# Kernel optimization log

Hardware: AMD Instinct MI355X
Metric: run time of the kernel (lower is better)

## Reference

```python
import jax, jax.numpy as jnp
import numpy as np
from jax import lax

NEG = -1e16  # value used by masked_fill in the original
DN = ('NCHW', 'OIHW', 'NCHW')


def _time_block(X, w1, b1, w2, b2, w3, b3):
    # X: [B, N, T, C] -> conv over time with kernel (1,3), VALID -> [B, N, T-2, O]
    x = jnp.transpose(X, (0, 3, 1, 2))  # [B, C, N, T]
    conv = lambda w, b: lax.conv_general_dilated(x, w, (1, 1), 'VALID', dimension_numbers=DN) + b[None, :, None, None]
    temp = conv(w1, b1) + jax.nn.sigmoid(conv(w2, b2))
    out = jax.nn.relu(temp + conv(w3, b3))
    return jnp.transpose(out, (0, 2, 3, 1))  # [B, N, T-2, O]


def _gat_single(x, graph, W, b):
    # x: [B, N, C]; W: [D, C]; b: [D]
    h = jnp.einsum('bnc,dc->bnd', x, W)
    s = jnp.einsum('bnd,bmd->bnm', h, h) * graph[None]
    s = jnp.where(s == 0, NEG, s)
    a = jax.nn.softmax(s, axis=-1)
    return jnp.einsum('bnm,bmd->bnd', a, h) + b


def _gat_multihead(x, graph, Wh, bh):
    # x: [B, N, C]; Wh: [H, D, C]; bh: [H, D] -> [B, N, H*D] (head-major concat, matching torch.cat)
    h = jnp.einsum('bnc,hdc->bhnd', x, Wh)
    s = jnp.einsum('bhnd,bhmd->bhnm', h, h) * graph[None, None]
    s = jnp.where(s == 0, NEG, s)
    a = jax.nn.softmax(s, axis=-1)
    o = jnp.einsum('bhnm,bhmd->bhnd', a, h) + bh[None, :, None, :]
    B, H, N, D = o.shape
    return jnp.transpose(o, (0, 2, 1, 3)).reshape(B, N, H * D)


def setup_inputs() -> dict:
    key = jax.random.key(0)
    ks = jax.random.split(key, 12)
    B, N, T, C = 2, 4096, 5, 192
    hid, out_c, H = 64, 64, 4
    inp = {
        'flow': jax.random.normal(ks[0], (B, N, T, C), jnp.float32),
        'graph': jax.random.randint(ks[1], (N, N), 0, 2).astype(jnp.float32),
        'tb_w1': jax.random.normal(ks[2], (hid, C, 1, 3), jnp.float32) * 0.1,
        'tb_b1': jax.random.normal(ks[3], (hid,), jnp.float32) * 0.1,
        'tb_w2': jax.random.normal(ks[4], (hid, C, 1, 3), jnp.float32) * 0.1,
        'tb_b2': jax.random.normal(ks[5], (hid,), jnp.float32) * 0.1,
        'tb_w3': jax.random.normal(ks[6], (hid, C, 1, 3), jnp.float32) * 0.1,
        'tb_b3': jax.random.normal(ks[7], (hid,), jnp.float32) * 0.1,
        'Wh': jax.random.normal(ks[8], (H, hid, C), jnp.float32) * 0.1,
        'bh': jax.random.normal(ks[9], (H, hid), jnp.float32) * 0.1,
        'Wo': jax.random.normal(ks[10], (out_c, hid * H), jnp.float32) * 0.1,
        'bo': jax.random.normal(ks[11], (out_c,), jnp.float32) * 0.1,
    }
    return inp


def reference(flow, graph, tb_w1, tb_b1, tb_w2, tb_b2, tb_w3, tb_b3, Wh, bh, Wo, bo):
    B, N = flow.shape[0], flow.shape[1]
    t1 = _time_block(flow, tb_w1, tb_b1, tb_w2, tb_b2, tb_w3, tb_b3)  # [B, N, T-2, hid]
    x = t1.reshape(B, N, -1)  # [B, N, (T-2)*hid]
    x = jax.nn.leaky_relu(_gat_multihead(x, graph, Wh, bh), negative_slope=0.01)
    x = jax.nn.leaky_relu(_gat_single(x, graph, Wo, bo), negative_slope=0.01)
    return x[:, :, None, :]  # [B, N, 1, out_c]
```

## Files before the change

### kernel.cpp

```cpp
#include <hip/hip_runtime.h>
#include <math.h>

#define N_NODES 4096

typedef unsigned short u16;
typedef unsigned int u32;

typedef __attribute__((ext_vector_type(8))) short bfrag;
typedef __attribute__((ext_vector_type(4))) float f4;

__device__ __forceinline__ u16 f2bf(float x) {
    union { float f; u32 u; } v; v.f = x;
    u32 r = (v.u + 0x7FFFu + ((v.u >> 16) & 1u)) >> 16;
    return (u16)r;
}
__device__ __forceinline__ float bf2f(u16 b) {
    union { float f; u32 u; } v; v.u = ((u32)b) << 16; return v.f;
}
__device__ __forceinline__ u32 cvtpk(float a, float b) {
    u32 r;
    asm("v_cvt_pk_bf16_f32 %0, %1, %2" : "=v"(r) : "v"(a), "v"(b));
    return r;
}
__device__ __forceinline__ float u2f(u32 u) {
    union { u32 u; float f; } v; v.u = u; return v.f;
}
__device__ __forceinline__ float fexp2(float x) {
    float r;
    asm("v_exp_f32 %0, %1" : "=v"(r) : "v"(x));
    return r;
}

#define LOG2E 1.4426950408889634f

__global__ __launch_bounds__(256) void wprep_kernel(
    const float* __restrict__ w1, const float* __restrict__ w2,
    const float* __restrict__ w3,
    u16* __restrict__ w_hi, u16* __restrict__ w_mid, u16* __restrict__ w_lo)
{
    int idx = blockIdx.x * 256 + threadIdx.x;
    if (idx >= 192 * 576) return;
    int col = idx / 576, k = idx % 576;
    int conv = col >> 6, o = col & 63;
    int kk = k / 192, c = k % 192;
    const float* w = (conv == 0) ? w1 : (conv == 1 ? w2 : w3);
    float v = w[(o * 192 + c) * 3 + kk];
    u16 h = f2bf(v);   float r1 = v - bf2f(h);
    u16 m = f2bf(r1);  float r2 = r1 - bf2f(m);
    u16 lo = f2bf(r2);
    int kc = k >> 6, rem = k & 63, j = rem >> 3, e = rem & 7;
    int pos = col * 576 + kc * 64 + ((j ^ (col & 7)) << 3) + e;
    w_hi[pos] = h;
    w_mid[pos] = m;
    w_lo[pos] = lo;
}

__global__ __launch_bounds__(512) void timeblock_mfma_kernel(
    const float* __restrict__ flow,
    const u16* __restrict__ w_hi, const u16* __restrict__ w_mid,
    const u16* __restrict__ w_lo,
    const float* __restrict__ b1, const float* __restrict__ b2,
    const float* __restrict__ b3, float* __restrict__ x1)
{
    __shared__ __align__(16) u16 As[3][128 * 64];
    __shared__ __align__(16) u16 Bs[3][192 * 64];

    const int tid = threadIdx.x;
    const int wv = tid >> 6, l = tid & 63;
    const int ln15 = l & 15, ln16 = l >> 4;
    const int wr = wv >> 1, wc = wv & 1;
    const int nodebase = blockIdx.x * 128;
    const int t = blockIdx.y;

    f4 acc[2][6];
#pragma unroll
    for (int rq = 0; rq < 2; ++rq)
#pragma unroll
        for (int nt = 0; nt < 6; ++nt) {
            acc[rq][nt][0] = 0.f; acc[rq][nt][1] = 0.f;
            acc[rq][nt][2] = 0.f; acc[rq][nt][3] = 0.f;
        }

    for (int kc = 0; kc < 9; ++kc) {
        __syncthreads();

#pragma unroll
        for (int u = tid; u < 1024; u += 512) {
            int r = u >> 3, j = u & 7;
            const float* srcp = flow + (size_t)(nodebase + r) * 960 + t * 192 + kc * 64 + j * 8;
            float4 f0 = *(const float4*)srcp;
            float4 f1 = *(const float4*)(srcp + 4);
            float fv[8] = { f0.x, f0.y, f0.z, f0.w, f1.x, f1.y, f1.z, f1.w };
            union { uint4 q; u16 a[8]; } uh, um, ul;
#pragma unroll
            for (int e = 0; e < 8; ++e) {
                u16 h = f2bf(fv[e]);   float r1 = fv[e] - bf2f(h);
                u16 m = f2bf(r1);      float r2 = r1 - bf2f(m);
                uh.a[e] = h; um.a[e] = m; ul.a[e] = f2bf(r2);
            }
            int pos = r * 64 + ((j ^ (r & 7)) << 3);
            *(uint4*)&As[0][pos] = uh.q;
            *(uint4*)&As[1][pos] = um.q;
            *(uint4*)&As[2][pos] = ul.q;
        }

#pragma unroll
        for (int arr = 0; arr < 3; ++arr) {
            const u16* wsrc = (arr == 0) ? w_hi : (arr == 1 ? w_mid : w_lo);
#pragma unroll
            for (int i = 0; i < 3; ++i) {
                int colg = wv * 24 + i * 8;
                const u16* srcp = wsrc + (size_t)(colg + (l >> 3)) * 576 + kc * 64 + (l & 7) * 8;
                u16* dstp = &Bs[arr][colg * 64];
                __builtin_amdgcn_global_load_lds(
                    (const __attribute__((address_space(1))) u32*)srcp,
                    (__attribute__((address_space(3))) u32*)dstp, 16, 0, 0);
            }
        }

        __syncthreads();

        bfrag af[2][3][2];
#pragma unroll
        for (int rq = 0; rq < 2; ++rq) {
            int arow = wr * 32 + rq * 16 + ln15;
#pragma unroll
            for (int ks = 0; ks < 2; ++ks) {
                int idx = arow * 64 + (((ks * 4 + ln16) ^ (arow & 7)) << 3);
                af[rq][0][ks] = *(const bfrag*)&As[0][idx];
                af[rq][1][ks] = *(const bfrag*)&As[1][idx];
                af[rq][2][ks] = *(const bfrag*)&As[2][idx];
            }
        }

#pragma unroll
        for (int cv = 0; cv < 3; ++cv) {
#pragma unroll
            for (int ntj = 0; ntj < 2; ++ntj) {
                int col = cv * 64 + wc * 32 + ntj * 16 + ln15;
                int nt = cv * 2 + ntj;
#pragma unroll
                for (int ks = 0; ks < 2; ++ks) {
                    int idx = col * 64 + (((ks * 4 + ln16) ^ (col & 7)) << 3);
                    bfrag bh = *(const bfrag*)&Bs[0][idx];
                    bfrag bm = *(const bfrag*)&Bs[1][idx];
                    bfrag bl = *(const bfrag*)&Bs[2][idx];
#pragma unroll
                    for (int rq = 0; rq < 2; ++rq) {
                        f4 a = acc[rq][nt];
                        a = __builtin_amdgcn_mfma_f32_16x16x32_bf16(af[rq][0][ks], bh, a, 0, 0, 0);
                        a = __builtin_amdgcn_mfma_f32_16x16x32_bf16(af[rq][0][ks], bm, a, 0, 0, 0);
                        a = __builtin_amdgcn_mfma_f32_16x16x32_bf16(af[rq][1][ks], bh, a, 0, 0, 0);
                        a = __builtin_amdgcn_mfma_f32_16x16x32_bf16(af[rq][0][ks], bl, a, 0, 0, 0);
                        a = __builtin_amdgcn_mfma_f32_16x16x32_bf16(af[rq][2][ks], bh, a, 0, 0, 0);
                        a = __builtin_amdgcn_mfma_f32_16x16x32_bf16(af[rq][1][ks], bm, a, 0, 0, 0);
                        acc[rq][nt] = a;
                    }
                }
            }
        }
    }

#pragma unroll
    for (int rq = 0; rq < 2; ++rq) {
#pragma unroll
        for (int ntj = 0; ntj < 2; ++ntj) {
            int o = wc * 32 + ntj * 16 + ln15;
            float bb1 = b1[o], bb2 = b2[o], bb3 = b3[o];
#pragma unroll
            for (int rg = 0; rg < 4; ++rg) {
                int node = nodebase + wr * 32 + rq * 16 + ln16 * 4 + rg;
                float c1 = acc[rq][0 * 2 + ntj][rg] + bb1;
                float c2 = acc[rq][1 * 2 + ntj][rg] + bb2;
                float c3 = acc[rq][2 * 2 + ntj][rg] + bb3;
                float sg = 1.0f / (1.0f + __expf(-c2));
                float v = c1 + sg + c3;
                x1[(size_t)node * 192 + t * 64 + o] = v > 0.f ? v : 0.f;
            }
        }
    }
}

__global__ __launch_bounds__(512) void linear_mfma_kernel(
    const float* __restrict__ in, const float* __restrict__ W,
    u16* __restrict__ h_hi, u16* __restrict__ h_lo,
    u16* __restrict__ hTb_hi, u16* __restrict__ hTb_lo,
    int C, int H, int nwc)
{
    __shared__ __align__(16) u16 As[3][256 * 64];
    __shared__ __align__(16) u16 Bs[3][128 * 64];

    const int tid = threadIdx.x;
    const int wv = tid >> 6, l = tid & 63;
    const int ln15 = l & 15, ln16 = l >> 4;
    const int wr = wv / nwc, wc = wv - wr * nwc;
    const int rows = 256 / nwc;
    const int ncol = 64 * nwc;
    const int rowbase = blockIdx.x * rows;
    const int colbase = blockIdx.y * ncol;

    f4 acc[2][4];
#pragma unroll
    for (int rq = 0; rq < 2; ++rq)
#pragma unroll
        for (int nt = 0; nt < 4; ++nt) {
            acc[rq][nt][0] = 0.f; acc[rq][nt][1] = 0.f;
            acc[rq][nt][2] = 0.f; acc[rq][nt][3] = 0.f;
        }

    const int nchunks = C >> 6;
    for (int kc = 0; kc < nchunks; ++kc) {
        __syncthreads();

        for (int u = tid; u < rows * 8; u += 512) {
            int r = u >> 3, j = u & 7;
            const float* srcp = in + (size_t)(rowbase + r) * C + kc * 64 + j * 8;
            float4 f0 = *(const float4*)srcp;
            float4 f1 = *(const float4*)(srcp + 4);
            float fv[8] = { f0.x, f0.y, f0.z, f0.w, f1.x, f1.y, f1.z, f1.w };
            union { uint4 q; u16 a[8]; } uh, um, ul;
#pragma unroll
            for (int e = 0; e < 8; ++e) {
                u16 h = f2bf(fv[e]);   float r1 = fv[e] - bf2f(h);
                u16 m = f2bf(r1);      float r2 = r1 - bf2f(m);
                uh.a[e] = h; um.a[e] = m; ul.a[e] = f2bf(r2);
            }
            int pos = r * 64 + ((j ^ (r & 7)) << 3);
            *(uint4*)&As[0][pos] = uh.q;
            *(uint4*)&As[1][pos] = um.q;
            *(uint4*)&As[2][pos] = ul.q;
        }

        for (int u = tid; u < ncol * 8; u += 512) {
            int cdx = u >> 3, j = u & 7;
            const float* srcp = W + (size_t)(colbase + cdx) * C + kc * 64 + j * 8;
            float4 f0 = *(const float4*)srcp;
            float4 f1 = *(const float4*)(srcp + 4);
            float fv[8] = { f0.x, f0.y, f0.z, f0.w, f1.x, f1.y, f1.z, f1.w };
            union { uint4 q; u16 a[8]; } uh, um, ul;
#pragma unroll
            for (int e = 0; e < 8; ++e) {
                u16 h = f2bf(fv[e]);   float r1 = fv[e] - bf2f(h);
                u16 m = f2bf(r1);      float r2 = r1 - bf2f(m);
                uh.a[e] = h; um.a[e] = m; ul.a[e] = f2bf(r2);
            }
            int pos = cdx * 64 + ((j ^ (cdx & 7)) << 3);
            *(uint4*)&Bs[0][pos] = uh.q;
            *(uint4*)&Bs[1][pos] = um.q;
            *(uint4*)&Bs[2][pos] = ul.q;
        }

        __syncthreads();

        bfrag af[2][3][2];
#pragma unroll
        for (int rq = 0; rq < 2; ++rq) {
            int arow = wr * 32 + rq * 16 + ln15;
#pragma unroll
            for (int ks = 0; ks < 2; ++ks) {
                int idx = arow * 64 + (((ks * 4 + ln16) ^ (arow & 7)) << 3);
                af[rq][0][ks] = *(const bfrag*)&As[0][idx];
                af[rq][1][ks] = *(const bfrag*)&As[1][idx];
                af[rq][2][ks] = *(const bfrag*)&As[2][idx];
            }
        }

#pragma unroll
        for (int nt = 0; nt < 4; ++nt) {
            int bcol = wc * 64 + nt * 16 + ln15;
#pragma unroll
            for (int ks = 0; ks < 2; ++ks) {
                int idx = bcol * 64 + (((ks * 4 + ln16) ^ (bcol & 7)) << 3);
                bfrag bh = *(const bfrag*)&Bs[0][idx];
                bfrag bm = *(const bfrag*)&Bs[1][idx];
                bfrag bl = *(const bfrag*)&Bs[2][idx];
#pragma unroll
                for (int rq = 0; rq < 2; ++rq) {
                    f4 a = acc[rq][nt];
                    a = __builtin_amdgcn_mfma_f32_16x16x32_bf16(af[rq][0][ks], bh, a, 0, 0, 0);
                    a = __builtin_amdgcn_mfma_f32_16x16x32_bf16(af[rq][0][ks], bm, a, 0, 0, 0);
                    a = __builtin_amdgcn_mfma_f32_16x16x32_bf16(af[rq][1][ks], bh, a, 0, 0, 0);
                    a = __builtin_amdgcn_mfma_f32_16x16x32_bf16(af[rq][0][ks], bl, a, 0, 0, 0);
                    a = __builtin_amdgcn_mfma_f32_16x16x32_bf16(af[rq][2][ks], bh, a, 0, 0, 0);
                    a = __builtin_amdgcn_mfma_f32_16x16x32_bf16(af[rq][1][ks], bm, a, 0, 0, 0);
                    acc[rq][nt] = a;
                }
            }
        }
    }

#pragma unroll
    for (int rq = 0; rq < 2; ++rq) {
#pragma unroll
        for (int nt = 0; nt < 4; ++nt) {
            int col = colbase + wc * 64 + nt * 16 + ln15;
            int g = col >> 6, d = col & 63;
            u16 hi4[4], lo4[4];
#pragma unroll
            for (int rg = 0; rg < 4; ++rg) {
                float a = acc[rq][nt][rg];
                u16 h = f2bf(a);
                hi4[rg] = h;
                lo4[rg] = f2bf(a - bf2f(h));
            }
            int row0 = rowbase + wr * 32 + rq * 16 + ln16 * 4;
            int b = row0 >> 12;
            int n0 = row0 & 4095;
            size_t mapb = (size_t)(b * H + g) * (4096 * 64);
#pragma unroll
            for (int rg = 0; rg < 4; ++rg) {
                h_hi[mapb + (size_t)(n0 + rg) * 64 + d] = hi4[rg];
                h_lo[mapb + (size_t)(n0 + rg) * 64 + d] = lo4[rg];
            }
            size_t tb = mapb + (size_t)(n0 >> 6) * 4096;
            ushort4 vh = { hi4[0], hi4[1], hi4[2], hi4[3] };
            ushort4 vl = { lo4[0], lo4[1], lo4[2], lo4[3] };
            *(ushort4*)&hTb_hi[tb + (size_t)d * 64 + (n0 & 63)] = vh;
            *(ushort4*)&hTb_lo[tb + (size_t)d * 64 + (n0 & 63)] = vl;
        }
    }
}

__global__ __launch_bounds__(256) void flash_mfma_kernel(
    const u16* __restrict__ h_hi, const u16* __restrict__ h_lo,
    const u16* __restrict__ hTb_hi, const u16* __restrict__ hTb_lo,
    const float* __restrict__ graph, const float* __restrict__ bias,
    float* __restrict__ out, int H, int rstride,
    int ntiles, int nch, int mode, float* __restrict__ pO, float* __restrict__ pml)
{
    __shared__ __align__(16) u16 Ks[2][2][4096];
    __shared__ __align__(16) u16 Vs[2][4096];

    const int tid = threadIdx.x;
    const int wv = tid >> 6;
    const int l = tid & 63;
    const int ln15 = l & 15, ln16 = l >> 4;
    const int bx = blockIdx.y;
    const int by = bx / nch;
    const int chunk = bx - by * nch;
    const int t0 = chunk * ntiles;
    const int bb = by / H, head = by - bb * H;
    const size_t mapb = (size_t)by * (4096 * 64);
    const int rowbase = blockIdx.x * 64;

    const int arow = rowbase + wv * 16 + ln15;
    bfrag ahi[2], alo[2];
#pragma unroll
    for (int ks = 0; ks < 2; ++ks) {
        ahi[ks] = *(const bfrag*)(h_hi + mapb + (size_t)arow * 64 + ks * 32 + ln16 * 8);
        alo[ks] = *(const bfrag*)(h_lo + mapb + (size_t)arow * 64 + ks * 32 + ln16 * 8);
    }

    const u16* gA = (wv == 0 ? h_hi : wv == 1 ? h_lo : wv == 2 ? hTb_hi : hTb_lo) + mapb;
    const int lrow = l >> 3;
    const int stoff = lrow * 64 + (((l & 7) ^ lrow) << 3);

#define STAGE_K(T, BUF)                                                        \
    if (wv < 2) {                                                              \
        const u16* srcp = gA + (size_t)(T) * 4096 + stoff;                     \
        u16* dstp = &Ks[BUF][wv][0];                                           \
        _Pragma("unroll")                                                      \
        for (int i_ = 0; i_ < 8; ++i_)                                         \
            __builtin_amdgcn_global_load_lds(                                  \
                (const __attribute__((address_space(1))) u32*)(srcp + i_ * 512), \
                (__attribute__((address_space(3))) u32*)(dstp + i_ * 512),     \
                16, 0, 0);                                                     \
    }
#define STAGE_V(T)                                                             \
    if (wv >= 2) {                                                             \
        const u16* srcp = gA + (size_t)(T) * 4096 + stoff;                     \
        u16* dstp = &Vs[wv - 2][0];                                            \
        _Pragma("unroll")                                                      \
        for (int i_ = 0; i_ < 8; ++i_)                                         \
            __builtin_amdgcn_global_load_lds(                                  \
                (const __attribute__((address_space(1))) u32*)(srcp + i_ * 512), \
                (__attribute__((address_space(3))) u32*)(dstp + i_ * 512),     \
                16, 0, 0);                                                     \
    }

    const float* grow = graph + (size_t)(rowbase + wv * 16 + ln15) * 4096 + ln16 * 4;

    float m_ = -3.0e38f, l_ = 0.f;
    f4 acco[4];
#pragma unroll
    for (int i = 0; i < 4; ++i) {
        acco[i][0] = 0.f; acco[i][1] = 0.f; acco[i][2] = 0.f; acco[i][3] = 0.f;
    }

    STAGE_K(t0, 0);
    float4 grC[4], grN[4];
#pragma unroll
    for (int cb = 0; cb < 4; ++cb)
        grC[cb] = *(const float4*)(grow + (size_t)t0 * 64 + cb * 16);

    const int srcA = ln15 + ((((ln16 << 1)) & 3) << 4);
    const int srcB = ln15 + ((((ln16 << 1) + 1) & 3) << 4);
    const bool hi2 = (ln16 & 2) != 0;

    for (int tt = 0; tt < ntiles; ++tt) {
        const int t = t0 + tt;
        const int cur = tt & 1;

        __syncthreads();

        STAGE_V(t);
        if (tt + 1 < ntiles) {
            STAGE_K(t + 1, cur ^ 1);
#pragma unroll
            for (int cb = 0; cb < 4; ++cb)
                grN[cb] = *(const float4*)(grow + (size_t)(t + 1) * 64 + cb * 16);
        }

        __builtin_amdgcn_s_setprio(1);
        f4 accs[4];
#pragma unroll
        for (int cb = 0; cb < 4; ++cb) {
            f4 a; a[0] = 0.f; a[1] = 0.f; a[2] = 0.f; a[3] = 0.f;
#pragma unroll
            for (int ks = 0; ks < 2; ++ks) {
                int c = cb * 16 + ln15;
                int idx = c * 64 + (((ks * 4 + ln16) * 8) ^ ((c & 7) << 3));
                bfrag bhi = *(const bfrag*)&Ks[cur][0][idx];
                bfrag blo = *(const bfrag*)&Ks[cur][1][idx];
                a = __builtin_amdgcn_mfma_f32_16x16x32_bf16(bhi, ahi[ks], a, 0, 0, 0);
                a = __builtin_amdgcn_mfma_f32_16x16x32_bf16(bhi, alo[ks], a, 0, 0, 0);
                a = __builtin_amdgcn_mfma_f32_16x16x32_bf16(blo, ahi[ks], a, 0, 0, 0);
            }
            accs[cb] = a;
        }
        __builtin_amdgcn_s_setprio(0);

        float p[4][4];
#pragma unroll
        for (int cb = 0; cb < 4; ++cb) {
            p[cb][0] = accs[cb][0] + fmaf(grC[cb].x, 1e16f, -1e16f);
            p[cb][1] = accs[cb][1] + fmaf(grC[cb].y, 1e16f, -1e16f);
            p[cb][2] = accs[cb][2] + fmaf(grC[cb].z, 1e16f, -1e16f);
            p[cb][3] = accs[cb][3] + fmaf(grC[cb].w, 1e16f, -1e16f);
        }

        float tm = fmaxf(fmaxf(p[0][0], p[0][1]), fmaxf(p[0][2], p[0][3]));
#pragma unroll
        for (int cb = 1; cb < 4; ++cb)
            tm = fmaxf(tm, fmaxf(fmaxf(p[cb][0], p[cb][1]), fmaxf(p[cb][2], p[cb][3])));
        tm = fmaxf(tm, __shfl_xor(tm, 16));
        tm = fmaxf(tm, __shfl_xor(tm, 32));

        const bool anyup = __any(tm > m_);
        float mn, corr;
        if (anyup) {
            mn = fmaxf(m_, tm);
            corr = fexp2((m_ - mn) * LOG2E);
        } else {
            mn = m_;
            corr = 1.0f;
        }
        const float c0 = -mn * LOG2E;

        float rs = 0.f;
#pragma unroll
        for (int cb = 0; cb < 4; ++cb) {
            p[cb][0] = fexp2(fmaf(p[cb][0], LOG2E, c0));
            p[cb][1] = fexp2(fmaf(p[cb][1], LOG2E, c0));
            p[cb][2] = fexp2(fmaf(p[cb][2], LOG2E, c0));
            p[cb][3] = fexp2(fmaf(p[cb][3], LOG2E, c0));
            rs += (p[cb][0] + p[cb][1]) + (p[cb][2] + p[cb][3]);
        }
        rs += __shfl_xor(rs, 16);
        rs += __shfl_xor(rs, 32);
        l_ = l_ * corr + rs;
        m_ = mn;

        if (anyup) {
            float corr4[4];
#pragma unroll
            for (int rg = 0; rg < 4; ++rg)
                corr4[rg] = __shfl(corr, ln16 * 4 + rg);
#pragma unroll
            for (int nb = 0; nb < 4; ++nb) {
                acco[nb][0] *= corr4[0]; acco[nb][1] *= corr4[1];
                acco[nb][2] *= corr4[2]; acco[nb][3] *= corr4[3];
            }
        }

        u32 Uh[4][2], Ul[4][2];
#pragma unroll
        for (int cb = 0; cb < 4; ++cb) {
            u32 uh0 = cvtpk(p[cb][0], p[cb][1]);
            u32 uh1 = cvtpk(p[cb][2], p[cb][3]);
            float h0 = u2f(uh0 << 16), h1 = u2f(uh0 & 0xffff0000u);
            float h2 = u2f(uh1 << 16), h3 = u2f(uh1 & 0xffff0000u);
            Uh[cb][0] = uh0; Uh[cb][1] = uh1;
            Ul[cb][0] = cvtpk(p[cb][0] - h0, p[cb][1] - h1);
            Ul[cb][1] = cvtpk(p[cb][2] - h2, p[cb][3] - h3);
        }

        bfrag pfh[2], pfl[2];
#pragma unroll
        for (int ks = 0; ks < 2; ++ks) {
            u32 w0a = (u32)__shfl((int)Uh[2 * ks + 0][0], srcA);
            u32 w0b = (u32)__shfl((int)Uh[2 * ks + 1][0], srcA);
            u32 w1a = (u32)__shfl((int)Uh[2 * ks + 0][1], srcA);
            u32 w1b = (u32)__shfl((int)Uh[2 * ks + 1][1], srcA);
            u32 w2a = (u32)__shfl((int)Uh[2 * ks + 0][0], srcB);
            u32 w2b = (u32)__shfl((int)Uh[2 * ks + 1][0], srcB);
            u32 w3a = (u32)__shfl((int)Uh[2 * ks + 0][1], srcB);
            u32 w3b = (u32)__shfl((int)Uh[2 * ks + 1][1], srcB);
            union { uint4 q; bfrag f; } ch;
            ch.q.x = hi2 ? w0b : w0a; ch.q.y = hi2 ? w1b : w1a;
            ch.q.z = hi2 ? w2b : w2a; ch.q.w = hi2 ? w3b : w3a;
            pfh[ks] = ch.f;

            u32 v0a = (u32)__shfl((int)Ul[2 * ks + 0][0], srcA);
            u32 v0b = (u32)__shfl((int)Ul[2 * ks + 1][0], srcA);
            u32 v1a = (u32)__shfl((int)Ul[2 * ks + 0][1], srcA);
            u32 v1b = (u32)__shfl((int)Ul[2 * ks + 1][1], srcA);
            u32 v2a = (u32)__shfl((int)Ul[2 * ks + 0][0], srcB);
            u32 v2b = (u32)__shfl((int)Ul[2 * ks + 1][0], srcB);
            u32 v3a = (u32)__shfl((int)Ul[2 * ks + 0][1], srcB);
            u32 v3b = (u32)__shfl((int)Ul[2 * ks + 1][1], srcB);
            union { uint4 q; bfrag f; } cl;
            cl.q.x = hi2 ? v0b : v0a; cl.q.y = hi2 ? v1b : v1a;
            cl.q.z = hi2 ? v2b : v2a; cl.q.w = hi2 ? v3b : v3a;
            pfl[ks] = cl.f;
        }

        __syncthreads();

        __builtin_amdgcn_s_setprio(1);
#pragma unroll
        for (int nb = 0; nb < 4; ++nb) {
#pragma unroll
            for (int ks = 0; ks < 2; ++ks) {
                int nr = nb * 16 + ln15;
                int idx = nr * 64 + (((ks * 4 + ln16) * 8) ^ ((nr & 7) << 3));
                bfrag vhi = *(const bfrag*)&Vs[0][idx];
                bfrag vlo = *(const bfrag*)&Vs[1][idx];
                acco[nb] = __builtin_amdgcn_mfma_f32_16x16x32_bf16(pfh[ks], vhi, acco[nb], 0, 0, 0);
                acco[nb] = __builtin_amdgcn_mfma_f32_16x16x32_bf16(pfh[ks], vlo, acco[nb], 0, 0, 0);
                acco[nb] = __builtin_amdgcn_mfma_f32_16x16x32_bf16(pfl[ks], vhi, acco[nb], 0, 0, 0);
            }
        }
        __builtin_amdgcn_s_setprio(0);

        if (tt + 1 < ntiles) {
#pragma unroll
            for (int cb = 0; cb < 4; ++cb)
                grC[cb] = grN[cb];
        }
    }
#undef STAGE_K
#undef STAGE_V

    if (mode == 0) {
        float l4[4];
#pragma unroll
        for (int rg = 0; rg < 4; ++rg)
            l4[rg] = __shfl(l_, ln16 * 4 + rg);

        const float* bv = bias + head * 64;
#pragma unroll
        for (int rg = 0; rg < 4; ++rg) {
            int row = rowbase + wv * 16 + ln16 * 4 + rg;
            float inv = 1.0f / l4[rg];
#pragma unroll
            for (int nb = 0; nb < 4; ++nb) {
                float v = acco[nb][rg] * inv + bv[nb * 16 + ln15];
                v = v > 0.f ? v : 0.01f * v;
                out[(size_t)(bb * N_NODES + row) * rstride + head * 64 + nb * 16 + ln15] = v;
            }
        }
    } else {
        int row = rowbase + wv * 16 + ln15;
        if (ln16 == 0) {
            size_t mi = (((size_t)(by * nch + chunk)) * 4096 + row) * 2;
            pml[mi] = m_;
            pml[mi + 1] = l_;
        }
#pragma unroll
        for (int rg = 0; rg < 4; ++rg) {
            int row2 = rowbase + wv * 16 + ln16 * 4 + rg;
            size_t ob = (((size_t)(by * nch + chunk)) * 4096 + row2) * 64;
#pragma unroll
            for (int nb = 0; nb < 4; ++nb)
                pO[ob + nb * 16 + ln15] = acco[nb][rg];
        }
    }
}

__global__ __launch_bounds__(256) void merge_kernel(
    const float* __restrict__ pO, const float* __restrict__ pml,
    const float* __restrict__ bias, float* __restrict__ out)
{
    int idx = blockIdx.x * 256 + threadIdx.x;
    int feat = idx & 63;
    int row = (idx >> 6) & 4095;
    int map = idx >> 18;

    float mv[4], lv[4];
    float M = -3.0e38f;
#pragma unroll
    for (int c = 0; c < 4; ++c) {
        size_t mi = (((size_t)map * 4 + c) * 4096 + row) * 2;
        mv[c] = pml[mi];
        lv[c] = pml[mi + 1];
        M = fmaxf(M, mv[c]);
    }
    float den = 0.f, num = 0.f;
#pragma unroll
    for (int c = 0; c < 4; ++c) {
        float e = __expf(mv[c] - M);
        den += e * lv[c];
        num += e * pO[(((size_t)map * 4 + c) * 4096 + row) * 64 + feat];
    }
    float v = num / den + bias[feat];
    v = v > 0.f ? v : 0.01f * v;
    out[((size_t)map * 4096 + row) * 64 + feat] = v;
}

extern "C" void kernel_launch(void* const* d_in, const int* in_sizes, int n_in,
                              void* d_out, int out_size, void* d_ws, size_t ws_size,
                              hipStream_t stream)
{
    const float* flow = (const float*)d_in[0];
    const float* graph = (const float*)d_in[1];
    const float* w1 = (const float*)d_in[2];
    const float* b1 = (const float*)d_in[3];
    const float* w2 = (const float*)d_in[4];
    const float* b2 = (const float*)d_in[5];
    const float* w3 = (const float*)d_in[6];
    const float* b3 = (const float*)d_in[7];
    const float* Wh = (const float*)d_in[8];
    const float* bh = (const float*)d_in[9];
    const float* Wo = (const float*)d_in[10];
    const float* bo = (const float*)d_in[11];

    char* ws = (char*)d_ws;
    u16* wc_hi  = (u16*)ws;
    u16* wc_mid = wc_hi + (size_t)192 * 576;
    u16* wc_lo  = wc_mid + (size_t)192 * 576;

    u16* h1_hi  = (u16*)ws;
    u16* h1_lo  = h1_hi + (size_t)8 * 4096 * 64;
    u16* h1T_hi = h1_lo + (size_t)8 * 4096 * 64;
    u16* h1T_lo = h1T_hi + (size_t)8 * 4096 * 64;
    u16* h2_hi  = (u16*)ws;
    u16* h2_lo  = h2_hi + (size_t)2 * 4096 * 64;
    u16* h2T_hi = h2_lo + (size_t)2 * 4096 * 64;
    u16* h2T_lo = h2T_hi + (size_t)2 * 4096 * 64;
    float* pml  = (float*)(ws + (size_t)6 * 1024 * 1024);
    float* xreg = (float*)(ws + (size_t)4 * 8 * 4096 * 64 * 2);
    float* x1 = xreg;
    float* x2 = xreg;
    float* pO = xreg;
    float* outp = (float*)d_out;

    hipLaunchKernelGGL(wprep_kernel, dim3(432), dim3(256), 0, stream,
                       w1, w2, w3, wc_hi, wc_mid, wc_lo);
    hipLaunchKernelGGL(timeblock_mfma_kernel, dim3(64, 3), dim3(512), 0, stream,
                       flow, wc_hi, wc_mid, wc_lo, b1, b2, b3, x1);
    hipLaunchKernelGGL(linear_mfma_kernel, dim3(64, 2), dim3(512), 0, stream,
                       x1, Wh, h1_hi, h1_lo, h1T_hi, h1T_lo, 192, 4, 2);
    hipLaunchKernelGGL(flash_mfma_kernel, dim3(64, 8), dim3(256), 0, stream,
                       h1_hi, h1_lo, h1T_hi, h1T_lo, graph, bh, x2, 4, 256,
                       64, 1, 0, (float*)nullptr, (float*)nullptr);
    hipLaunchKernelGGL(linear_mfma_kernel, dim3(32, 1), dim3(512), 0, stream,
                       x2, Wo, h2_hi, h2_lo, h2T_hi, h2T_lo, 256, 1, 1);
    hipLaunchKernelGGL(flash_mfma_kernel, dim3(64, 8), dim3(256), 0, stream,
                       h2_hi, h2_lo, h2T_hi, h2T_lo, graph, bo, (float*)nullptr, 1, 64,
                       16, 4, 1, pO, pml);
    hipLaunchKernelGGL(merge_kernel, dim3(2048), dim3(256), 0, stream,
                       pO, pml, bo, outp);
}
```

Measured before the change: 303.7 us.

## Add dedicated single-head flash kernel with finer key split for second GAT layer

Replaces the generic flash kernel for the single-head second attention layer with a specialised kernel. It uses direct global-to-LDS loads, a register-prefetched graph mask, and a skipped rescale when the running max does not change. The key dimension is split into 8 chunks instead of 4, doubling the grid to raise occupancy. The merge kernel now takes the chunk count as a parameter, and the partial buffers move to a new workspace region, so merge traffic grows.

```diff
diff --git a/kernel.cpp b/kernel.cpp
--- a/kernel.cpp
+++ b/kernel.cpp
@@ -588,30 +588,273 @@
     }
 }
 
+__global__ __launch_bounds__(256) void flash1s_kernel(
+    const u16* __restrict__ h_hi, const u16* __restrict__ h_lo,
+    const u16* __restrict__ hTb_hi, const u16* __restrict__ hTb_lo,
+    const float* __restrict__ graph,
+    int H, int ntiles, int nch, float* __restrict__ pO, float* __restrict__ pml)
+{
+    __shared__ __align__(16) u16 Ks[2][4096];
+    __shared__ __align__(16) u16 Vs[2][4096];
+
+    const int tid = threadIdx.x;
+    const int wv = tid >> 6;
+    const int l = tid & 63;
+    const int ln15 = l & 15, ln16 = l >> 4;
+    const int bx = blockIdx.y;
+    const int by = bx / nch;
+    const int chunk = bx - by * nch;
+    const int t0 = chunk * ntiles;
+    const size_t mapb = (size_t)by * (4096 * 64);
+    const int rowbase = blockIdx.x * 64;
+
+    const int arow = rowbase + wv * 16 + ln15;
+    bfrag ahi[2], alo[2];
+#pragma unroll
+    for (int ks = 0; ks < 2; ++ks) {
+        ahi[ks] = *(const bfrag*)(h_hi + mapb + (size_t)arow * 64 + ks * 32 + ln16 * 8);
+        alo[ks] = *(const bfrag*)(h_lo + mapb + (size_t)arow * 64 + ks * 32 + ln16 * 8);
+    }
+
+    const u16* gA = (wv == 0 ? h_hi : wv == 1 ? h_lo : wv == 2 ? hTb_hi : hTb_lo) + mapb;
+    const int lrow = l >> 3;
+    const int stoff = lrow * 64 + (((l & 7) ^ lrow) << 3);
+
+#define STAGE_K1(T)                                                            \
+    if (wv < 2) {                                                              \
+        const u16* srcp = gA + (size_t)(T) * 4096 + stoff;                     \
+        u16* dstp = &Ks[wv][0];                                                \
+        _Pragma("unroll")                                                      \
+        for (int i_ = 0; i_ < 8; ++i_)                                         \
+            __builtin_amdgcn_global_load_lds(                                  \
+                (const __attribute__((address_space(1))) u32*)(srcp + i_ * 512), \
+                (__attribute__((address_space(3))) u32*)(dstp + i_ * 512),     \
+                16, 0, 0);                                                     \
+    }
+#define STAGE_V1(T)                                                            \
+    if (wv >= 2) {                                                             \
+        const u16* srcp = gA + (size_t)(T) * 4096 + stoff;                     \
+        u16* dstp = &Vs[wv - 2][0];                                            \
+        _Pragma("unroll")                                                      \
+        for (int i_ = 0; i_ < 8; ++i_)                                         \
+            __builtin_amdgcn_global_load_lds(                                  \
+                (const __attribute__((address_space(1))) u32*)(srcp + i_ * 512), \
+                (__attribute__((address_space(3))) u32*)(dstp + i_ * 512),     \
+                16, 0, 0);                                                     \
+    }
+
+    const float* grow = graph + (size_t)(rowbase + wv * 16 + ln15) * 4096 + ln16 * 4;
+
+    float m_ = -3.0e38f, l_ = 0.f;
+    f4 acco[4];
+#pragma unroll
+    for (int i = 0; i < 4; ++i) {
+        acco[i][0] = 0.f; acco[i][1] = 0.f; acco[i][2] = 0.f; acco[i][3] = 0.f;
+    }
+
+    STAGE_K1(t0);
+    float4 grC[4], grN[4];
+#pragma unroll
+    for (int cb = 0; cb < 4; ++cb)
+        grC[cb] = *(const float4*)(grow + (size_t)t0 * 64 + cb * 16);
+
+    const int srcA = ln15 + ((((ln16 << 1)) & 3) << 4);
+    const int srcB = ln15 + ((((ln16 << 1) + 1) & 3) << 4);
+    const bool hi2 = (ln16 & 2) != 0;
+
+    for (int tt = 0; tt < ntiles; ++tt) {
+        const int t = t0 + tt;
+
+        __syncthreads();
+
+        STAGE_V1(t);
+
+        __builtin_amdgcn_s_setprio(1);
+        f4 accs[4];
+#pragma unroll
+        for (int cb = 0; cb < 4; ++cb) {
+            f4 a; a[0] = 0.f; a[1] = 0.f; a[2] = 0.f; a[3] = 0.f;
+#pragma unroll
+            for (int ks = 0; ks < 2; ++ks) {
+                int c = cb * 16 + ln15;
+                int idx = c * 64 + (((ks * 4 + ln16) * 8) ^ ((c & 7) << 3));
+                bfrag bhi = *(const bfrag*)&Ks[0][idx];
+                bfrag blo = *(const bfrag*)&Ks[1][idx];
+                a = __builtin_amdgcn_mfma_f32_16x16x32_bf16(bhi, ahi[ks], a, 0, 0, 0);
+                a = __builtin_amdgcn_mfma_f32_16x16x32_bf16(bhi, alo[ks], a, 0, 0, 0);
+                a = __builtin_amdgcn_mfma_f32_16x16x32_bf16(blo, ahi[ks], a, 0, 0, 0);
+            }
+            accs[cb] = a;
+        }
+        __builtin_amdgcn_s_setprio(0);
+
+        __syncthreads();
+
+        if (tt + 1 < ntiles) {
+            STAGE_K1(t + 1);
+#pragma unroll
+            for (int cb = 0; cb < 4; ++cb)
+                grN[cb] = *(const float4*)(grow + (size_t)(t + 1) * 64 + cb * 16);
+        }
+
+        float p[4][4];
+#pragma unroll
+        for (int cb = 0; cb < 4; ++cb) {
+            p[cb][0] = accs[cb][0] + fmaf(grC[cb].x, 1e16f, -1e16f);
+            p[cb][1] = accs[cb][1] + fmaf(grC[cb].y, 1e16f, -1e16f);
+            p[cb][2] = accs[cb][2] + fmaf(grC[cb].z, 1e16f, -1e16f);
+            p[cb][3] = accs[cb][3] + fmaf(grC[cb].w, 1e16f, -1e16f);
+        }
+
+        float tm = fmaxf(fmaxf(p[0][0], p[0][1]), fmaxf(p[0][2], p[0][3]));
+#pragma unroll
+        for (int cb = 1; cb < 4; ++cb)
+            tm = fmaxf(tm, fmaxf(fmaxf(p[cb][0], p[cb][1]), fmaxf(p[cb][2], p[cb][3])));
+        tm = fmaxf(tm, __shfl_xor(tm, 16));
+        tm = fmaxf(tm, __shfl_xor(tm, 32));
+
+        const bool anyup = __any(tm > m_);
+        float mn, corr;
+        if (anyup) {
+            mn = fmaxf(m_, tm);
+            corr = fexp2((m_ - mn) * LOG2E);
+        } else {
+            mn = m_;
+            corr = 1.0f;
+        }
+        const float c0 = -mn * LOG2E;
+
+        float rs = 0.f;
+#pragma unroll
+        for (int cb = 0; cb < 4; ++cb) {
+            p[cb][0] = fexp2(fmaf(p[cb][0], LOG2E, c0));
+            p[cb][1] = fexp2(fmaf(p[cb][1], LOG2E, c0));
+            p[cb][2] = fexp2(fmaf(p[cb][2], LOG2E, c0));
+            p[cb][3] = fexp2(fmaf(p[cb][3], LOG2E, c0));
+            rs += (p[cb][0] + p[cb][1]) + (p[cb][2] + p[cb][3]);
+        }
+        rs += __shfl_xor(rs, 16);
+        rs += __shfl_xor(rs, 32);
+        l_ = l_ * corr + rs;
+        m_ = mn;
+
+        if (anyup) {
+            float corr4[4];
+#pragma unroll
+            for (int rg = 0; rg < 4; ++rg)
+                corr4[rg] = __shfl(corr, ln16 * 4 + rg);
+#pragma unroll
+            for (int nb = 0; nb < 4; ++nb) {
+                acco[nb][0] *= corr4[0]; acco[nb][1] *= corr4[1];
+                acco[nb][2] *= corr4[2]; acco[nb][3] *= corr4[3];
+            }
+        }
+
+        u32 Uh[4][2], Ul[4][2];
+#pragma unroll
+        for (int cb = 0; cb < 4; ++cb) {
+            u32 uh0 = cvtpk(p[cb][0], p[cb][1]);
+            u32 uh1 = cvtpk(p[cb][2], p[cb][3]);
+            float h0 = u2f(uh0 << 16), h1 = u2f(uh0 & 0xffff0000u);
+            float h2 = u2f(uh1 << 16), h3 = u2f(uh1 & 0xffff0000u);
+            Uh[cb][0] = uh0; Uh[cb][1] = uh1;
+            Ul[cb][0] = cvtpk(p[cb][0] - h0, p[cb][1] - h1);
+            Ul[cb][1] = cvtpk(p[cb][2] - h2, p[cb][3] - h3);
+        }
+
+        bfrag pfh[2], pfl[2];
+#pragma unroll
+        for (int ks = 0; ks < 2; ++ks) {
+            u32 w0a = (u32)__shfl((int)Uh[2 * ks + 0][0], srcA);
+            u32 w0b = (u32)__shfl((int)Uh[2 * ks + 1][0], srcA);
+            u32 w1a = (u32)__shfl((int)Uh[2 * ks + 0][1], srcA);
+            u32 w1b = (u32)__shfl((int)Uh[2 * ks + 1][1], srcA);
+            u32 w2a = (u32)__shfl((int)Uh[2 * ks + 0][0], srcB);
+            u32 w2b = (u32)__shfl((int)Uh[2 * ks + 1][0], srcB);
+            u32 w3a = (u32)__shfl((int)Uh[2 * ks + 0][1], srcB);
+            u32 w3b = (u32)__shfl((int)Uh[2 * ks + 1][1], srcB);
+            union { uint4 q; bfrag f; } ch;
+            ch.q.x = hi2 ? w0b : w0a; ch.q.y = hi2 ? w1b : w1a;
+            ch.q.z = hi2 ? w2b : w2a; ch.q.w = hi2 ? w3b : w3a;
+            pfh[ks] = ch.f;
+
+            u32 v0a = (u32)__shfl((int)Ul[2 * ks + 0][0], srcA);
+            u32 v0b = (u32)__shfl((int)Ul[2 * ks + 1][0], srcA);
+            u32 v1a = (u32)__shfl((int)Ul[2 * ks + 0][1], srcA);
+            u32 v1b = (u32)__shfl((int)Ul[2 * ks + 1][1], srcA);
+            u32 v2a = (u32)__shfl((int)Ul[2 * ks + 0][0], srcB);
+            u32 v2b = (u32)__shfl((int)Ul[2 * ks + 1][0], srcB);
+            u32 v3a = (u32)__shfl((int)Ul[2 * ks + 0][1], srcB);
+            u32 v3b = (u32)__shfl((int)Ul[2 * ks + 1][1], srcB);
+            union { uint4 q; bfrag f; } cl;
+            cl.q.x = hi2 ? v0b : v0a; cl.q.y = hi2 ? v1b : v1a;
+            cl.q.z = hi2 ? v2b : v2a; cl.q.w = hi2 ? v3b : v3a;
+            pfl[ks] = cl.f;
+        }
+
+        __syncthreads();
+
+        __builtin_amdgcn_s_setprio(1);
+#pragma unroll
+        for (int nb = 0; nb < 4; ++nb) {
+#pragma unroll
+            for (int ks = 0; ks < 2; ++ks) {
+                int nr = nb * 16 + ln15;
+                int idx = nr * 64 + (((ks * 4 + ln16) * 8) ^ ((nr & 7) << 3));
+                bfrag vhi = *(const bfrag*)&Vs[0][idx];
+                bfrag vlo = *(const bfrag*)&Vs[1][idx];
+                acco[nb] = __builtin_amdgcn_mfma_f32_16x16x32_bf16(pfh[ks], vhi, acco[nb], 0, 0, 0);
+                acco[nb] = __builtin_amdgcn_mfma_f32_16x16x32_bf16(pfh[ks], vlo, acco[nb], 0, 0, 0);
+                acco[nb] = __builtin_amdgcn_mfma_f32_16x16x32_bf16(pfl[ks], vhi, acco[nb], 0, 0, 0);
+            }
+        }
+        __builtin_amdgcn_s_setprio(0);
+
+        if (tt + 1 < ntiles) {
+#pragma unroll
+            for (int cb = 0; cb < 4; ++cb)
+                grC[cb] = grN[cb];
+        }
+    }
+#undef STAGE_K1
+#undef STAGE_V1
+
+    int row = rowbase + wv * 16 + ln15;
+    if (ln16 == 0) {
+        size_t mi = (((size_t)(by * nch + chunk)) * 4096 + row) * 2;
+        pml[mi] = m_;
+        pml[mi + 1] = l_;
+    }
+#pragma unroll
+    for (int rg = 0; rg < 4; ++rg) {
+        int row2 = rowbase + wv * 16 + ln16 * 4 + rg;
+        size_t ob = (((size_t)(by * nch + chunk)) * 4096 + row2) * 64;
+#pragma unroll
+        for (int nb = 0; nb < 4; ++nb)
+            pO[ob + nb * 16 + ln15] = acco[nb][rg];
+    }
+}
+
 __global__ __launch_bounds__(256) void merge_kernel(
     const float* __restrict__ pO, const float* __restrict__ pml,
-    const float* __restrict__ bias, float* __restrict__ out)
+    const float* __restrict__ bias, float* __restrict__ out, int nch)
 {
     int idx = blockIdx.x * 256 + threadIdx.x;
     int feat = idx & 63;
     int row = (idx >> 6) & 4095;
     int map = idx >> 18;
 
-    float mv[4], lv[4];
     float M = -3.0e38f;
-#pragma unroll
-    for (int c = 0; c < 4; ++c) {
-        size_t mi = (((size_t)map * 4 + c) * 4096 + row) * 2;
-        mv[c] = pml[mi];
-        lv[c] = pml[mi + 1];
-        M = fmaxf(M, mv[c]);
+    for (int c = 0; c < nch; ++c) {
+        size_t mi = (((size_t)map * nch + c) * 4096 + row) * 2;
+        M = fmaxf(M, pml[mi]);
     }
     float den = 0.f, num = 0.f;
-#pragma unroll
-    for (int c = 0; c < 4; ++c) {
-        float e = __expf(mv[c] - M);
-        den += e * lv[c];
-        num += e * pO[(((size_t)map * 4 + c) * 4096 + row) * 64 + feat];
+    for (int c = 0; c < nch; ++c) {
+        size_t mi = (((size_t)map * nch + c) * 4096 + row) * 2;
+        float e = __expf(pml[mi] - M);
+        den += e * pml[mi + 1];
+        num += e * pO[(((size_t)map * nch + c) * 4096 + row) * 64 + feat];
     }
     float v = num / den + bias[feat];
     v = v > 0.f ? v : 0.01f * v;
@@ -648,11 +891,11 @@
     u16* h2_lo  = h2_hi + (size_t)2 * 4096 * 64;
     u16* h2T_hi = h2_lo + (size_t)2 * 4096 * 64;
     u16* h2T_lo = h2T_hi + (size_t)2 * 4096 * 64;
-    float* pml  = (float*)(ws + (size_t)6 * 1024 * 1024);
     float* xreg = (float*)(ws + (size_t)4 * 8 * 4096 * 64 * 2);
     float* x1 = xreg;
     float* x2 = xreg;
-    float* pO = xreg;
+    float* pO  = (float*)(ws + (size_t)4 * 2 * 4096 * 64 * 2);
+    float* pml = (float*)(ws + (size_t)4 * 2 * 4096 * 64 * 2 + (size_t)16 * 4096 * 64 * 4);
     float* outp = (float*)d_out;
 
     hipLaunchKernelGGL(wprep_kernel, dim3(432), dim3(256), 0, stream,
@@ -666,9 +909,9 @@
                        64, 1, 0, (float*)nullptr, (float*)nullptr);
     hipLaunchKernelGGL(linear_mfma_kernel, dim3(32, 1), dim3(512), 0, stream,
                        x2, Wo, h2_hi, h2_lo, h2T_hi, h2T_lo, 256, 1, 1);
-    hipLaunchKernelGGL(flash_mfma_kernel, dim3(64, 8), dim3(256), 0, stream,
-                       h2_hi, h2_lo, h2T_hi, h2T_lo, graph, bo, (float*)nullptr, 1, 64,
-                       16, 4, 1, pO, pml);
+    hipLaunchKernelGGL(flash1s_kernel, dim3(64, 16), dim3(256), 0, stream,
+                       h2_hi, h2_lo, h2T_hi, h2T_lo, graph,
+                       1, 8, 8, pO, pml);
     hipLaunchKernelGGL(merge_kernel, dim3(2048), dim3(256), 0, stream,
-                       pO, pml, bo, outp);
-}
+                       pO, pml, bo, outp, 8);
+}
```

Result: slower. 309.8 us (+2.0%).
